# Kernel tuning notes

Measured on AMD Instinct MI355X. Metric: run time of the kernel, lower is better.

## Reference

```python
import jax, jax.numpy as jnp
import numpy as np

B, C_IN, H, W = 8, 256, 32, 32
DK = 256
DV = 256
NH = 8
DKH = DK // NH  # 32
C_OUT = 512
KS, PAD = 3, 1


def setup_inputs() -> dict:
    key = jax.random.key(0)
    ks = jax.random.split(key, 9)
    s = 0.05
    return {
        "x": jax.random.normal(ks[0], (B, C_IN, H, W), jnp.float32),
        "w_qkv": jax.random.normal(ks[1], (2 * DK + DV, C_IN, 1, 1), jnp.float32) * s,
        "b_qkv": jnp.zeros((2 * DK + DV,), jnp.float32),
        "w_attn": jax.random.normal(ks[2], (DV, DV, 1, 1), jnp.float32) * s,
        "b_attn": jnp.zeros((DV,), jnp.float32),
        "w_out": jax.random.normal(ks[3], (C_OUT - DV, C_IN, KS, KS), jnp.float32) * s,
        "b_out": jnp.zeros((C_OUT - DV,), jnp.float32),
        # torch init: dkh**-0.5 + rand
        "key_rel_w": DKH ** (-0.5) + jax.random.uniform(ks[4], (2 * W - 1, DKH), jnp.float32),
        "key_rel_h": DKH ** (-0.5) + jax.random.uniform(ks[5], (2 * H - 1, DKH), jnp.float32),
    }


def conv2d(x, w, b, pad):
    y = jax.lax.conv_general_dilated(
        x, w, window_strides=(1, 1), padding=[(pad, pad), (pad, pad)],
        dimension_numbers=("NCHW", "OIHW", "NCHW"))
    return y + b[None, :, None, None]


def rel_to_abs(x):
    # x: [b, nh, L, 2L-1] -> [b, nh, L, L] (skew trick)
    b, nh, L, _ = x.shape
    x = jnp.pad(x, ((0, 0), (0, 0), (0, 0), (0, 1)))
    flat = x.reshape(b, nh, L * 2 * L)
    flat = jnp.pad(flat, ((0, 0), (0, 0), (0, L - 1)))
    final = flat.reshape(b, nh, L + 1, 2 * L - 1)
    return final[:, :, :L, L - 1:]


def relative_logits_1d(q, rel_k, Hd, Wd, transpose_mask):
    # q: [B, NH, DKH, Hd, Wd]; rel_k: [2*Wd-1, DKH]
    rel = jnp.einsum("bhdxy,md->bhxym", q, rel_k)          # [B,NH,Hd,Wd,2Wd-1]
    rel = rel.reshape(-1, NH * Hd, Wd, 2 * Wd - 1)
    rel = rel_to_abs(rel)                                   # [B,NH*Hd,Wd,Wd]
    rel = rel.reshape(-1, NH, Hd, 1, Wd, Wd)
    rel = jnp.broadcast_to(rel, (rel.shape[0], NH, Hd, Hd, Wd, Wd))
    rel = jnp.transpose(rel, transpose_mask)
    return rel.reshape(-1, NH, Hd * Wd, Hd * Wd)


def reference(x, w_qkv, b_qkv, w_attn, b_attn, w_out, b_out, key_rel_w, key_rel_h):
    conv_out = conv2d(x, w_out, b_out, PAD)                 # [B, C_OUT-DV, H, W]
    qkv = conv2d(x, w_qkv, b_qkv, 0)                        # [B, 2DK+DV, H, W]
    q, k, v = jnp.split(qkv, [DK, 2 * DK], axis=1)
    q = q.reshape(B, NH, DKH, H * W) * (DKH ** -0.5)        # scaled BEFORE rel logits (as in torch)
    k = k.reshape(B, NH, DKH, H * W)
    v = v.reshape(B, NH, DV // NH, H * W)
    logits = jnp.einsum("bhdl,bhdm->bhlm", q, k)            # [B,NH,HW,HW]
    q5 = q.reshape(B, NH, DKH, H, W)
    w_rel = relative_logits_1d(q5, key_rel_w, H, W, (0, 1, 2, 4, 3, 5))
    h_rel = relative_logits_1d(jnp.transpose(q5, (0, 1, 2, 4, 3)), key_rel_h, W, H, (0, 1, 4, 2, 5, 3))
    logits = logits + h_rel + w_rel
    weights = jax.nn.softmax(logits, axis=-1)
    attn = jnp.einsum("bhlm,bhdm->bhdl", weights, v)        # [B,NH,DVH,HW]
    attn = attn.reshape(B, DV, H, W)
    attn = conv2d(attn, w_attn, b_attn, 0)
    return jnp.concatenate([conv_out, attn], axis=1)        # [B, C_OUT, H, W]
```

## Files before the change

### kernel.cpp

```cpp
#include <hip/hip_runtime.h>
#include <hip/hip_bf16.h>


typedef __hip_bfloat16 bf16;
typedef __attribute__((ext_vector_type(8))) short bf16x8;
typedef __attribute__((ext_vector_type(4))) float f32x4;

__device__ __forceinline__ float bf2f(bf16 v) { return __bfloat162float(v); }
__device__ __forceinline__ float blo(unsigned int v) { return __uint_as_float(v << 16); }
__device__ __forceinline__ float bhi(unsigned int v) { return __uint_as_float(v & 0xffff0000u); }
__device__ __forceinline__ unsigned short f2bfbits(float f) {
  union { bf16 h; unsigned short u; } cv; cv.h = __float2bfloat16(f); return cv.u;
}
__device__ __forceinline__ unsigned int cvt_pk_bf16(float lo, float hi) {
  unsigned int r;
  asm("v_cvt_pk_bf16_f32 %0, %1, %2" : "=v"(r) : "v"(lo), "v"(hi));
  return r;
}
__device__ __forceinline__ float exp2_f(float x) {
#if __has_builtin(__builtin_amdgcn_exp2f)
  return __builtin_amdgcn_exp2f(x);
#else
  return exp2f(x);
#endif
}

__global__ __launch_bounds__(256) void prep_kernel(
    const float* __restrict__ x, const float* __restrict__ wout,
    bf16* __restrict__ xT, bf16* __restrict__ wob0, bf16* __restrict__ wob1)
{
  int bid = blockIdx.x, tid = threadIdx.x;
  if (bid < 2048) {
    __shared__ float t[32 * 33];
    int b = bid >> 8, rem = bid & 255;
    int ci0 = (rem >> 5) * 32, l0 = (rem & 31) * 32;
    {
      int ciL = tid >> 3, lL4 = (tid & 7) * 4;
      float4 v = *(const float4*)(x + (size_t)(b * 256 + ci0 + ciL) * 1024 + l0 + lL4);
      t[ciL * 33 + lL4 + 0] = v.x; t[ciL * 33 + lL4 + 1] = v.y;
      t[ciL * 33 + lL4 + 2] = v.z; t[ciL * 33 + lL4 + 3] = v.w;
    }
    __syncthreads();
    {
      int lL = tid >> 3, cS = (tid & 7) * 4;
      unsigned int p0 = (unsigned int)f2bfbits(t[(cS + 0) * 33 + lL]) |
                        ((unsigned int)f2bfbits(t[(cS + 1) * 33 + lL]) << 16);
      unsigned int p1 = (unsigned int)f2bfbits(t[(cS + 2) * 33 + lL]) |
                        ((unsigned int)f2bfbits(t[(cS + 3) * 33 + lL]) << 16);
      uint2 u2; u2.x = p0; u2.y = p1;
      *(uint2*)(xT + ((size_t)(b * 1024) + l0 + lL) * 256 + ci0 + cS) = u2;
    }
  } else {
    int t0 = (bid - 2048) * 256 + tid;
#pragma unroll
    for (int s = 0; s < 8; ++s) {
      int u = s * 9216 + t0;
      int chunkblk = u / 2304;
      int within = u - chunkblk * 2304;
      int co63 = within / 36;
      int r = within - co63 * 36;
      int kidx = r >> 2, cig = r & 3;
      int co = (chunkblk >> 3) * 64 + co63;
      int ci = (chunkblk & 7) * 32 + cig * 8;
      union { unsigned short h[8]; uint4 u4; } pk;
#pragma unroll
      for (int j = 0; j < 8; ++j)
        pk.h[j] = f2bfbits(wout[(size_t)(co * 256 + ci + j) * 9 + kidx]);
      bf16* dst = (chunkblk < 28) ? (wob0 + (size_t)chunkblk * 18432)
                                  : (wob1 + (size_t)(chunkblk - 28) * 18432);
      *(uint4*)(dst + (size_t)within * 8) = pk.u4;
    }
  }
}

__global__ __launch_bounds__(256) void convqkv_kernel(
    const bf16* __restrict__ xT,
    const bf16* __restrict__ wob0, const bf16* __restrict__ wob1,
    const float* __restrict__ b_out, float* __restrict__ out,
    const float* __restrict__ wq, const float* __restrict__ b_qkv,
    bf16* __restrict__ qT, bf16* __restrict__ kR, bf16* __restrict__ vW)
{
  __shared__ __align__(16) short smem[27104];
  int tid = threadIdx.x, lane = tid & 63, wave = tid >> 6;
  int m16 = lane & 15, quad = lane >> 4;

  if (blockIdx.x < 256) {
    short* wS = smem;
    short* xS = smem + 18944;
    int bid = blockIdx.x;
    int rc = bid & 7, cotile = (bid >> 3) & 3, b = bid >> 5;
    int y0 = rc * 4;

    f32x4 acc[8];
#pragma unroll
    for (int t = 0; t < 8; ++t) acc[t] = (f32x4){0.f, 0.f, 0.f, 0.f};

    for (int ck = 0; ck < 8; ++ck) {
      __syncthreads();
      int cb = cotile * 8 + ck;
      const bf16* wbase = (cb < 28) ? (wob0 + (size_t)cb * 18432)
                                    : (wob1 + (size_t)(cb - 28) * 18432);
#pragma unroll
      for (int r = 0; r < 9; ++r) {
        int u = r * 256 + tid;
        *(uint4*)(wS + (u / 36) * 296 + (u % 36) * 8) = *(const uint4*)(wbase + (size_t)u * 8);
      }
#pragma unroll
      for (int r = 0; r < 3; ++r) {
        int u = r * 256 + tid;
        int pos = u >> 2, seg = u & 3;
        int row = pos >> 5, col = pos & 31;
        int gy = y0 - 1 + row;
        uint4 val = make_uint4(0u, 0u, 0u, 0u);
        if (gy >= 0 && gy < 32)
          val = *(const uint4*)(xT + ((size_t)(b * 1024) + gy * 32 + col) * 256 + ck * 32 + seg * 8);
        *(uint4*)(xS + (row * 34 + col + 1) * 40 + seg * 8) = val;
      }
      if (tid < 48) {
        int pos = tid >> 2, seg = tid & 3;
        int row = pos >> 1, side = pos & 1;
        *(uint4*)(xS + (row * 34 + side * 33) * 40 + seg * 8) = make_uint4(0u, 0u, 0u, 0u);
      }
      __syncthreads();
#pragma unroll
      for (int kidx = 0; kidx < 9; ++kidx) {
        int dy = kidx / 3, dx = kidx - dy * 3;
        bf16x8 af = *(const bf16x8*)(wS + (wave * 16 + m16) * 296 + kidx * 32 + quad * 8);
#pragma unroll
        for (int t = 0; t < 8; ++t) {
          int row = (t >> 1) + dy;
          int col = (t & 1) * 16 + m16 + dx;
          bf16x8 bf = *(const bf16x8*)(xS + (row * 34 + col) * 40 + quad * 8);
          acc[t] = __builtin_amdgcn_mfma_f32_16x16x32_bf16(af, bf, acc[t], 0, 0, 0);
        }
      }
    }

    int cob = cotile * 64 + wave * 16 + quad * 4;
#pragma unroll
    for (int i = 0; i < 4; ++i) {
      float bv = b_out[cob + i];
#pragma unroll
      for (int t = 0; t < 8; ++t) {
        int y = y0 + (t >> 1), xc = (t & 1) * 16 + m16;
        out[((size_t)(b * 512) + cob + i) * 1024 + y * 32 + xc] = acc[t][i] + bv;
      }
    }
  } else {
    short* aS = smem;
    short* bS = smem + 4608;
    int bid2 = blockIdx.x - 256;
    int ltile = bid2 & 7;
    int rest = bid2 >> 3;
    int ctile = rest % 12;
    int b = rest / 12;
    int l0 = ltile * 128;
    int cbase = ctile * 64;

    f32x4 acc[8];
#pragma unroll
    for (int t = 0; t < 8; ++t) acc[t] = (f32x4){0.f, 0.f, 0.f, 0.f};

    for (int ck = 0; ck < 4; ++ck) {
      __syncthreads();
#pragma unroll
      for (int r = 0; r < 4; ++r) {
        int u = r * 256 + tid;
        int c = u >> 4, s4 = u & 15;
        float4 v = *(const float4*)(wq + (size_t)(cbase + c) * 256 + ck * 64 + s4 * 4);
        unsigned int p0 = (unsigned int)f2bfbits(v.x) | ((unsigned int)f2bfbits(v.y) << 16);
        unsigned int p1 = (unsigned int)f2bfbits(v.z) | ((unsigned int)f2bfbits(v.w) << 16);
        uint2 u2; u2.x = p0; u2.y = p1;
        *(uint2*)(aS + c * 72 + s4 * 4) = u2;
      }
#pragma unroll
      for (int r = 0; r < 4; ++r) {
        int u = r * 256 + tid;
        int l = u >> 3, seg = u & 7;
        *(uint4*)(bS + l * 72 + seg * 8) =
            *(const uint4*)(xT + ((size_t)(b * 1024) + l0 + l) * 256 + ck * 64 + seg * 8);
      }
      __syncthreads();
#pragma unroll
      for (int ks = 0; ks < 2; ++ks) {
        bf16x8 af = *(const bf16x8*)(aS + (wave * 16 + m16) * 72 + ks * 32 + quad * 8);
#pragma unroll
        for (int t = 0; t < 8; ++t) {
          bf16x8 bf = *(const bf16x8*)(bS + (t * 16 + m16) * 72 + ks * 32 + quad * 8);
          acc[t] = __builtin_amdgcn_mfma_f32_16x16x32_bf16(af, bf, acc[t], 0, 0, 0);
        }
      }
    }

    __syncthreads();
    short* ldsT = smem + wave * 3072;
    int cb = cbase + wave * 16;
    bool isq = (ctile < 4);
    float bv[4];
#pragma unroll
    for (int i = 0; i < 4; ++i) bv[i] = b_qkv[cb + quad * 4 + i];
#pragma unroll
    for (int t = 0; t < 8; ++t) {
#pragma unroll
      for (int i = 0; i < 4; ++i) {
        float v = acc[t][i] + bv[i];
        if (isq) v *= 0.17677669529663689f;
        ldsT[(t * 16 + m16) * 24 + quad * 4 + i] = (short)f2bfbits(v);
      }
    }
    if (ctile < 8) {
      bf16* dst = isq ? qT : kR;
      int coff = isq ? cb : cb - 256;
#pragma unroll
      for (int rep = 0; rep < 4; ++rep) {
        int u = rep * 64 + lane;
        int l = u >> 1, half = u & 1;
        int c0 = coff + half * 8;
        int head = b * 8 + (c0 >> 5), d0 = c0 & 31;
        *(uint4*)(dst + ((size_t)head * 1024 + l0 + l) * 32 + d0) =
            *(const uint4*)(ldsT + l * 24 + half * 8);
      }
    } else {
      int dcol = lane >> 2, lg = lane & 3;
      int c2 = (cb - 512) + dcol;
      int head = b * 8 + (c2 >> 5), gd = c2 & 31;
#pragma unroll
      for (int s = 0; s < 4; ++s) {
        union { unsigned int w[4]; uint4 u4; } pk;
#pragma unroll
        for (int p = 0; p < 4; ++p) {
          int j0 = lg * 32 + s * 8 + p * 2;
          unsigned int u0 = (unsigned short)ldsT[j0 * 24 + dcol];
          unsigned int u1 = (unsigned short)ldsT[(j0 + 1) * 24 + dcol];
          pk.w[p] = u0 | (u1 << 16);
        }
        *(uint4*)(vW + ((size_t)head * 32 + gd) * 1024 + l0 + lg * 32 + s * 8) = pk.u4;
      }
    }
  }
}

__global__ __launch_bounds__(256) void attn_mfma_kernel(
    const bf16* __restrict__ qT, const bf16* __restrict__ kR, const bf16* __restrict__ vW,
    const float* __restrict__ krw, const float* __restrict__ krh,
    bf16* __restrict__ attL)
{
  __shared__ __align__(16) char smem[37376];
  short* kS0 = (short*)smem;
  short* kS1 = (short*)(smem + 5120);
  short* vt0 = (short*)(smem + 10240);
  short* vt1 = (short*)(smem + 14848);
  float* stgF = (float*)smem;
  float* rhS  = (float*)(smem + 19456);
  float* rwS  = (float*)(smem + 28160);

  const float L2E = 1.4426950408889634f;

  int tid = threadIdx.x;
  int lane = tid & 63, wave = tid >> 6;
  int m16 = lane & 15, quad = lane >> 4;
  int bid = blockIdx.x;
  int head = ((bid & 7) << 3) | ((bid >> 3) & 7);
  int qt = bid >> 6;
  int row0 = qt * 64;
  int b = head >> 3, h = head & 7;

  int skey = tid >> 2, sseg = tid & 3;
  int svd = tid >> 3, svk = tid & 7;
  const bf16* kptr = kR + (size_t)head * 32768 + skey * 32 + sseg * 8;
  const bf16* vptr = vW + (size_t)head * 32768 + svd * 1024 + svk * 8;
  uint4 kreg = *(const uint4*)kptr;
  uint4 vreg = *(const uint4*)vptr;

  int r = tid >> 2, jseg = tid & 3;
  float q32[32];
  {
    const bf16* qp = qT + ((size_t)head * 1024 + row0 + r) * 32;
#pragma unroll
    for (int s4 = 0; s4 < 4; ++s4) {
      uint4 u = ((const uint4*)qp)[s4];
      q32[s4 * 8 + 0] = blo(u.x); q32[s4 * 8 + 1] = bhi(u.x);
      q32[s4 * 8 + 2] = blo(u.y); q32[s4 * 8 + 3] = bhi(u.y);
      q32[s4 * 8 + 4] = blo(u.z); q32[s4 * 8 + 5] = bhi(u.z);
      q32[s4 * 8 + 6] = blo(u.w); q32[s4 * 8 + 7] = bhi(u.w);
    }
  }

  for (int i = tid; i < 504; i += 256) {
    int row = i >> 3, d0 = (i & 7) * 4;
    *(float4*)(stgF + row * 36 + d0) = *(const float4*)(krw + row * 32 + d0);
  }
  __syncthreads();

  {
    int qi = r & 31;
#pragma unroll
    for (int jj2 = 0; jj2 < 2; ++jj2) {
      float rv[4];
#pragma unroll
      for (int jp = 0; jp < 4; ++jp) {
        int j = jseg * 8 + jj2 * 4 + jp;
        const float* kw = stgF + (j - qi + 31) * 36;
        float s1 = 0.f;
#pragma unroll
        for (int d4 = 0; d4 < 8; ++d4) {
          float4 kv = *(const float4*)(kw + d4 * 4);
          s1 += q32[d4 * 4 + 0] * kv.x + q32[d4 * 4 + 1] * kv.y +
                q32[d4 * 4 + 2] * kv.z + q32[d4 * 4 + 3] * kv.w;
        }
        rv[jp] = s1 * L2E;
      }
      *(float4*)(rwS + r * 36 + jseg * 8 + jj2 * 4) = make_float4(rv[0], rv[1], rv[2], rv[3]);
    }
  }
  __syncthreads();

  for (int i = tid; i < 504; i += 256) {
    int row = i >> 3, d0 = (i & 7) * 4;
    *(float4*)(stgF + row * 36 + d0) = *(const float4*)(krh + row * 32 + d0);
  }
  __syncthreads();

  {
    int qx = qt * 2 + (r >> 5);
#pragma unroll
    for (int jj = 0; jj < 8; ++jj) {
      int j = jseg * 8 + jj;
      const float* kh = stgF + (j - qx + 31) * 36;
      float s2 = 0.f;
#pragma unroll
      for (int d4 = 0; d4 < 8; ++d4) {
        float4 kv = *(const float4*)(kh + d4 * 4);
        s2 += q32[d4 * 4 + 0] * kv.x + q32[d4 * 4 + 1] * kv.y +
              q32[d4 * 4 + 2] * kv.z + q32[d4 * 4 + 3] * kv.w;
      }
      rhS[j * 68 + r] = s2 * L2E;
    }
  }
  __syncthreads();

  bf16x8 afrag = *(const bf16x8*)(
      qT + ((size_t)head * 1024 + row0 + wave * 16 + m16) * 32 + quad * 8);
  float rwreg[2][4];
  {
    float4 rw0 = *(const float4*)(rwS + (wave * 16 + m16) * 36 + quad * 4);
    float4 rw1 = *(const float4*)(rwS + (wave * 16 + m16) * 36 + 16 + quad * 4);
    rwreg[0][0] = rw0.x; rwreg[0][1] = rw0.y; rwreg[0][2] = rw0.z; rwreg[0][3] = rw0.w;
    rwreg[1][0] = rw1.x; rwreg[1][1] = rw1.y; rwreg[1][2] = rw1.z; rwreg[1][3] = rw1.w;
  }

  *(uint4*)(kS0 + skey * 40 + sseg * 8) = kreg;
  *(uint4*)(vt0 + svd * 72 + svk * 8) = vreg;
  kreg = *(const uint4*)(kptr + 2048);
  vreg = *(const uint4*)(vptr + 64);

  f32x4 oacc[2];
  oacc[0] = (f32x4){0.f, 0.f, 0.f, 0.f};
  oacc[1] = (f32x4){0.f, 0.f, 0.f, 0.f};
  float rsp = 0.f;

  for (int c = 0; c < 16; ++c) {
    __syncthreads();
    if (c < 15) {
      short* kN = (c & 1) ? kS0 : kS1;
      short* vN = (c & 1) ? vt0 : vt1;
      *(uint4*)(kN + skey * 40 + sseg * 8) = kreg;
      *(uint4*)(vN + svd * 72 + svk * 8) = vreg;
      if (c < 14) {
        kreg = *(const uint4*)(kptr + (c + 2) * 2048);
        vreg = *(const uint4*)(vptr + (c + 2) * 64);
      }
    }
    const short* kC = (c & 1) ? kS1 : kS0;
    const short* vC = (c & 1) ? vt1 : vt0;

    float rh0 = rhS[(c * 2 + 0) * 68 + wave * 16 + m16];
    float rh1 = rhS[(c * 2 + 1) * 68 + wave * 16 + m16];

    f32x4 sacc[4];
#pragma unroll
    for (int t = 0; t < 4; ++t) {
      bf16x8 kf = *(const bf16x8*)(kC + (t * 16 + m16) * 40 + quad * 8);
      f32x4 z = (f32x4){0.f, 0.f, 0.f, 0.f};
      sacc[t] = __builtin_amdgcn_mfma_f32_16x16x32_bf16(kf, afrag, z, 0, 0, 0);
    }

    unsigned int pk[4][2];
#pragma unroll
    for (int t = 0; t < 4; ++t) {
      float rh = (t < 2) ? rh0 : rh1;
      float e[4];
#pragma unroll
      for (int i = 0; i < 4; ++i) {
        e[i] = exp2_f(fmaf(sacc[t][i], L2E, rwreg[t & 1][i] + rh));
        rsp += e[i];
      }
      pk[t][0] = cvt_pk_bf16(e[0], e[1]);
      pk[t][1] = cvt_pk_bf16(e[2], e[3]);
    }

#pragma unroll
    for (int ks = 0; ks < 2; ++ks) {
      union { unsigned int w[4]; bf16x8 v; } pf;
      pf.w[0] = pk[2 * ks][0];     pf.w[1] = pk[2 * ks][1];
      pf.w[2] = pk[2 * ks + 1][0]; pf.w[3] = pk[2 * ks + 1][1];
#pragma unroll
      for (int dt = 0; dt < 2; ++dt) {
        const short* vb = vC + (dt * 16 + m16) * 72 + ks * 32 + quad * 4;
        union { uint2 u[2]; bf16x8 v; } vf;
        vf.u[0] = *(const uint2*)(vb);
        vf.u[1] = *(const uint2*)(vb + 16);
        oacc[dt] = __builtin_amdgcn_mfma_f32_16x16x32_bf16(vf.v, pf.v, oacc[dt], 0, 0, 0);
      }
    }
  }

  rsp += __shfl_xor(rsp, 16, 64);
  rsp += __shfl_xor(rsp, 32, 64);
  float invs = 1.0f / rsp;
  int grow = row0 + wave * 16 + m16;
#pragma unroll
  for (int dt = 0; dt < 2; ++dt) {
    uint2 st;
    st.x = cvt_pk_bf16(oacc[dt][0] * invs, oacc[dt][1] * invs);
    st.y = cvt_pk_bf16(oacc[dt][2] * invs, oacc[dt][3] * invs);
    *(uint2*)(attL + ((size_t)b * 1024 + grow) * 256 + h * 32 + dt * 16 + quad * 4) = st;
  }
}

__global__ __launch_bounds__(256) void attnout_mfma_kernel(
    const bf16* __restrict__ attL, const float* __restrict__ w, const float* __restrict__ bias,
    float* __restrict__ out)
{
  __shared__ __align__(16) short smem[13824];
  short* aS = smem;
  short* bS = smem + 4608;

  int tid = threadIdx.x, lane = tid & 63, wave = tid >> 6;
  int m16 = lane & 15, quad = lane >> 4;
  int l0 = blockIdx.x * 128;
  int cotile = blockIdx.y;
  int b = blockIdx.z;
  int cbase = cotile * 64;

  f32x4 acc[8];
#pragma unroll
  for (int t = 0; t < 8; ++t) acc[t] = (f32x4){0.f, 0.f, 0.f, 0.f};

  for (int ck = 0; ck < 4; ++ck) {
    __syncthreads();
#pragma unroll
    for (int r = 0; r < 4; ++r) {
      int u = r * 256 + tid;
      int c = u >> 4, s4 = u & 15;
      float4 v = *(const float4*)(w + (size_t)(cbase + c) * 256 + ck * 64 + s4 * 4);
      unsigned int p0 = (unsigned int)f2bfbits(v.x) | ((unsigned int)f2bfbits(v.y) << 16);
      unsigned int p1 = (unsigned int)f2bfbits(v.z) | ((unsigned int)f2bfbits(v.w) << 16);
      uint2 u2; u2.x = p0; u2.y = p1;
      *(uint2*)(aS + c * 72 + s4 * 4) = u2;
    }
#pragma unroll
    for (int r = 0; r < 4; ++r) {
      int u = r * 256 + tid;
      int l = u >> 3, seg = u & 7;
      *(uint4*)(bS + l * 72 + seg * 8) =
          *(const uint4*)(attL + ((size_t)(b * 1024) + l0 + l) * 256 + ck * 64 + seg * 8);
    }
    __syncthreads();
#pragma unroll
    for (int ks = 0; ks < 2; ++ks) {
      bf16x8 af = *(const bf16x8*)(aS + (wave * 16 + m16) * 72 + ks * 32 + quad * 8);
#pragma unroll
      for (int t = 0; t < 8; ++t) {
        bf16x8 bf = *(const bf16x8*)(bS + (t * 16 + m16) * 72 + ks * 32 + quad * 8);
        acc[t] = __builtin_amdgcn_mfma_f32_16x16x32_bf16(af, bf, acc[t], 0, 0, 0);
      }
    }
  }

  int co = cbase + wave * 16 + quad * 4;
#pragma unroll
  for (int i = 0; i < 4; ++i) {
    float bv = bias[co + i];
    size_t obase = ((size_t)(b * 512) + 256 + co + i) * 1024 + l0;
#pragma unroll
    for (int t = 0; t < 8; ++t)
      out[obase + t * 16 + m16] = acc[t][i] + bv;
  }
}

extern "C" void kernel_launch(void* const* d_in, const int* in_sizes, int n_in,
                              void* d_out, int out_size, void* d_ws, size_t ws_size,
                              hipStream_t stream) {
  const float* x      = (const float*)d_in[0];
  const float* w_qkv  = (const float*)d_in[1];
  const float* b_qkv  = (const float*)d_in[2];
  const float* w_attn = (const float*)d_in[3];
  const float* b_attn = (const float*)d_in[4];
  const float* w_out  = (const float*)d_in[5];
  const float* b_out  = (const float*)d_in[6];
  const float* krw    = (const float*)d_in[7];
  const float* krh    = (const float*)d_in[8];
  float* out = (float*)d_out;

  bf16* ws    = (bf16*)d_ws;
  bf16* xT    = ws;
  bf16* attL  = ws;
  bf16* qT    = ws + 2097152;
  bf16* kR    = ws + 4194304;
  bf16* vW    = ws + 6291456;

  bf16* wob0 = (bf16*)(out + (size_t)(0 * 512 + 256) * 1024);
  bf16* wob1 = (bf16*)(out + (size_t)(1 * 512 + 256) * 1024);

  prep_kernel<<<dim3(2084), 256, 0, stream>>>(x, w_out, xT, wob0, wob1);
  convqkv_kernel<<<dim3(1024), 256, 0, stream>>>(xT, wob0, wob1, b_out, out,
                                                 w_qkv, b_qkv, qT, kR, vW);
  attn_mfma_kernel<<<dim3(1024), 256, 0, stream>>>(qT, kR, vW, krw, krh, attL);
  attnout_mfma_kernel<<<dim3(8, 4, 8), 256, 0, stream>>>(attL, w_attn, b_attn, out);
}
```

Before: 150.0 us.

## Load K/V MFMA fragments directly from global memory, dropping LDS staging

The attention kernel no longer stages K and V tiles through double-buffered shared memory with per-chunk block barriers. Each lane now reads its MFMA operand fragments straight from global memory (relying on L1/L2 since K/V per head is reused by all query tiles). This removes the LDS writes and the __syncthreads in the 16-iteration loop and shrinks shared memory, which can raise occupancy. The cost is more, less coalesced global loads (V reads are 8-byte pieces) with latency that is now exposed unless the compiler hoists them. It also changes the row-sum accumulation to a tree order.

```diff
diff --git a/kernel.cpp b/kernel.cpp
--- a/kernel.cpp
+++ b/kernel.cpp
@@ -6,7 +6,6 @@
 typedef __attribute__((ext_vector_type(8))) short bf16x8;
 typedef __attribute__((ext_vector_type(4))) float f32x4;
 
-__device__ __forceinline__ float bf2f(bf16 v) { return __bfloat162float(v); }
 __device__ __forceinline__ float blo(unsigned int v) { return __uint_as_float(v << 16); }
 __device__ __forceinline__ float bhi(unsigned int v) { return __uint_as_float(v & 0xffff0000u); }
 __device__ __forceinline__ unsigned short f2bfbits(float f) {
@@ -245,14 +244,10 @@
     const float* __restrict__ krw, const float* __restrict__ krh,
     bf16* __restrict__ attL)
 {
-  __shared__ __align__(16) char smem[37376];
-  short* kS0 = (short*)smem;
-  short* kS1 = (short*)(smem + 5120);
-  short* vt0 = (short*)(smem + 10240);
-  short* vt1 = (short*)(smem + 14848);
+  __shared__ __align__(16) char smem[27648];
   float* stgF = (float*)smem;
-  float* rhS  = (float*)(smem + 19456);
-  float* rwS  = (float*)(smem + 28160);
+  float* rhS  = (float*)(smem + 9728);
+  float* rwS  = (float*)(smem + 18432);
 
   const float L2E = 1.4426950408889634f;
 
@@ -265,13 +260,6 @@
   int row0 = qt * 64;
   int b = head >> 3, h = head & 7;
 
-  int skey = tid >> 2, sseg = tid & 3;
-  int svd = tid >> 3, svk = tid & 7;
-  const bf16* kptr = kR + (size_t)head * 32768 + skey * 32 + sseg * 8;
-  const bf16* vptr = vW + (size_t)head * 32768 + svd * 1024 + svk * 8;
-  uint4 kreg = *(const uint4*)kptr;
-  uint4 vreg = *(const uint4*)vptr;
-
   int r = tid >> 2, jseg = tid & 3;
   float q32[32];
   {
@@ -322,11 +310,11 @@
   __syncthreads();
 
   {
-    int qx = qt * 2 + (r >> 5);
+    int qy = qt * 2 + (r >> 5);
 #pragma unroll
     for (int jj = 0; jj < 8; ++jj) {
       int j = jseg * 8 + jj;
-      const float* kh = stgF + (j - qx + 31) * 36;
+      const float* kh = stgF + (j - qy + 31) * 36;
       float s2 = 0.f;
 #pragma unroll
       for (int d4 = 0; d4 < 8; ++d4) {
@@ -349,10 +337,8 @@
     rwreg[1][0] = rw1.x; rwreg[1][1] = rw1.y; rwreg[1][2] = rw1.z; rwreg[1][3] = rw1.w;
   }
 
-  *(uint4*)(kS0 + skey * 40 + sseg * 8) = kreg;
-  *(uint4*)(vt0 + svd * 72 + svk * 8) = vreg;
-  kreg = *(const uint4*)(kptr + 2048);
-  vreg = *(const uint4*)(vptr + 64);
+  const bf16* kp = kR + (size_t)head * 32768 + m16 * 32 + quad * 8;
+  const bf16* vp = vW + (size_t)head * 32768 + m16 * 1024 + quad * 4;
 
   f32x4 oacc[2];
   oacc[0] = (f32x4){0.f, 0.f, 0.f, 0.f};
@@ -360,27 +346,13 @@
   float rsp = 0.f;
 
   for (int c = 0; c < 16; ++c) {
-    __syncthreads();
-    if (c < 15) {
-      short* kN = (c & 1) ? kS0 : kS1;
-      short* vN = (c & 1) ? vt0 : vt1;
-      *(uint4*)(kN + skey * 40 + sseg * 8) = kreg;
-      *(uint4*)(vN + svd * 72 + svk * 8) = vreg;
-      if (c < 14) {
-        kreg = *(const uint4*)(kptr + (c + 2) * 2048);
-        vreg = *(const uint4*)(vptr + (c + 2) * 64);
-      }
-    }
-    const short* kC = (c & 1) ? kS1 : kS0;
-    const short* vC = (c & 1) ? vt1 : vt0;
-
     float rh0 = rhS[(c * 2 + 0) * 68 + wave * 16 + m16];
     float rh1 = rhS[(c * 2 + 1) * 68 + wave * 16 + m16];
 
     f32x4 sacc[4];
 #pragma unroll
     for (int t = 0; t < 4; ++t) {
-      bf16x8 kf = *(const bf16x8*)(kC + (t * 16 + m16) * 40 + quad * 8);
+      bf16x8 kf = *(const bf16x8*)(kp + c * 2048 + t * 512);
       f32x4 z = (f32x4){0.f, 0.f, 0.f, 0.f};
       sacc[t] = __builtin_amdgcn_mfma_f32_16x16x32_bf16(kf, afrag, z, 0, 0, 0);
     }
@@ -389,14 +361,13 @@
 #pragma unroll
     for (int t = 0; t < 4; ++t) {
       float rh = (t < 2) ? rh0 : rh1;
-      float e[4];
-#pragma unroll
-      for (int i = 0; i < 4; ++i) {
-        e[i] = exp2_f(fmaf(sacc[t][i], L2E, rwreg[t & 1][i] + rh));
-        rsp += e[i];
-      }
-      pk[t][0] = cvt_pk_bf16(e[0], e[1]);
-      pk[t][1] = cvt_pk_bf16(e[2], e[3]);
+      float e0 = exp2_f(fmaf(sacc[t][0], L2E, rwreg[t & 1][0] + rh));
+      float e1 = exp2_f(fmaf(sacc[t][1], L2E, rwreg[t & 1][1] + rh));
+      float e2 = exp2_f(fmaf(sacc[t][2], L2E, rwreg[t & 1][2] + rh));
+      float e3 = exp2_f(fmaf(sacc[t][3], L2E, rwreg[t & 1][3] + rh));
+      rsp += (e0 + e1) + (e2 + e3);
+      pk[t][0] = cvt_pk_bf16(e0, e1);
+      pk[t][1] = cvt_pk_bf16(e2, e3);
     }
 
 #pragma unroll
@@ -406,7 +377,7 @@
       pf.w[2] = pk[2 * ks + 1][0]; pf.w[3] = pk[2 * ks + 1][1];
 #pragma unroll
       for (int dt = 0; dt < 2; ++dt) {
-        const short* vb = vC + (dt * 16 + m16) * 72 + ks * 32 + quad * 4;
+        const bf16* vb = vp + dt * 16384 + c * 64 + ks * 32;
         union { uint2 u[2]; bf16x8 v; } vf;
         vf.u[0] = *(const uint2*)(vb);
         vf.u[1] = *(const uint2*)(vb + 16);
```

Measured after the change: 194.0 us. +29.3%, slower.
